# Kernel tuning notes

Measured on AMD Instinct MI355X. Metric: run time of the kernel, lower is better.

The kernel has to match this reference:

```python
import jax, jax.numpy as jnp
import numpy as np

N = 100000
IN_DIM = 256
HID = 128
E = 1600000


def _gcn_conv(x, W, b, src, dst, n_nodes):
    """PyG GCNConv: add self-loops, symmetric normalization, linear transform."""
    xw = x @ W  # [N, H]
    loop = jnp.arange(n_nodes, dtype=src.dtype)
    s = jnp.concatenate([src, loop])  # sources (j)
    d = jnp.concatenate([dst, loop])  # targets (i)
    ones = jnp.ones(s.shape[0], dtype=x.dtype)
    deg = jax.ops.segment_sum(ones, d, num_segments=n_nodes)  # in-degree incl. self-loop
    dinv = jnp.where(deg > 0, jax.lax.rsqrt(deg), 0.0)
    norm = dinv[s] * dinv[d]  # [E+N]
    msgs = xw[s] * norm[:, None]  # gather + scale
    out = jax.ops.segment_sum(msgs, d, num_segments=n_nodes)  # scatter-add at targets
    return out + b


def setup_inputs() -> dict:
    key = jax.random.key(0)
    ks = jax.random.split(key, 12)
    x = jax.random.normal(ks[0], (N, IN_DIM), dtype=jnp.float32)
    edge_index = jax.random.randint(ks[1], (2, E), 0, N, dtype=jnp.int64)
    h_node = jax.random.uniform(ks[2], (N,), dtype=jnp.float32)
    # learned params (glorot-ish scale)
    W1 = jax.random.normal(ks[3], (IN_DIM, HID), dtype=jnp.float32) / np.sqrt(IN_DIM)
    b1 = jnp.zeros((HID,), dtype=jnp.float32)
    W2 = jax.random.normal(ks[4], (HID, HID), dtype=jnp.float32) / np.sqrt(HID)
    b2 = jnp.zeros((HID,), dtype=jnp.float32)
    Wc = jax.random.normal(ks[5], (HID, 2), dtype=jnp.float32) / np.sqrt(HID)
    bc = jnp.zeros((2,), dtype=jnp.float32)
    Wf = jax.random.normal(ks[6], (HID, 2), dtype=jnp.float32) / np.sqrt(HID)
    bf = jnp.zeros((2,), dtype=jnp.float32)
    return {"x": x, "edge_index": edge_index, "h_node": h_node,
            "W1": W1, "b1": b1, "W2": W2, "b2": b2,
            "Wc": Wc, "bc": bc, "Wf": Wf, "bf": bf}


def reference(x, edge_index, h_node, W1, b1, W2, b2, Wc, bc, Wf, bf):
    src, dst = edge_index[0], edge_index[1]
    h1 = jax.nn.relu(_gcn_conv(x, W1, b1, src, dst, x.shape[0]))      # [N, HID]
    logits_coarse = h1 @ Wc + bc                                      # [N, 2]
    alpha = h_node[:, None]                                           # [N, 1]
    h2 = jax.nn.relu(_gcn_conv(h1, W2, b2, src, dst, x.shape[0]))     # [N, HID]
    h2_adaptive = alpha * h2 + (1.0 - alpha) * h1
    logits_fine = h2_adaptive @ Wf + bf                               # [N, 2]
    return 0.5 * logits_coarse + 0.5 * logits_fine
```

## Files before the change

kernel.cpp:

```cpp
#include <hip/hip_runtime.h>


#define HID 128
#define SHIFT 9
#define RANGE 512
#define MAXB 256
#define TILE 4096

typedef __bf16 bf16x8 __attribute__((ext_vector_type(8)));
typedef float  f32x4  __attribute__((ext_vector_type(4)));
typedef float  f32x2  __attribute__((ext_vector_type(2)));

__device__ __forceinline__ unsigned short f2bf(float x) {
    unsigned int b = __float_as_uint(x);
    b += 0x7fffu + ((b >> 16) & 1u);
    return (unsigned short)(b >> 16);
}
__device__ __forceinline__ float bflo(unsigned int u) { return __uint_as_float(u << 16); }
__device__ __forceinline__ float bfhi(unsigned int u) { return __uint_as_float(u & 0xffff0000u); }
__device__ __forceinline__ unsigned packbf(float a, float b) {
    return (unsigned)f2bf(a) | ((unsigned)f2bf(b) << 16);
}


__global__ __launch_bounds__(256)
void bincount_kernel(const int* __restrict__ dst, int* __restrict__ bin_counts,
                     int E, int NB) {
    __shared__ int h[MAXB];
    for (int i = threadIdx.x; i < NB; i += 256) h[i] = 0;
    __syncthreads();
    const int base = blockIdx.x * TILE;
#pragma unroll
    for (int j = 0; j < TILE; j += 256) {
        int e = base + j + threadIdx.x;
        if (e < E) atomicAdd(&h[((unsigned)dst[e]) >> SHIFT], 1);
    }
    __syncthreads();
    for (int i = threadIdx.x; i < NB; i += 256) {
        int v = h[i];
        if (v) atomicAdd(&bin_counts[i], v);
    }
}

__global__ void binscan_kernel(const int* __restrict__ bin_counts,
                               int* __restrict__ bin_off, int* __restrict__ bin_cur, int NB) {
    __shared__ int sh[MAXB];
    const int t = threadIdx.x;
    int v = (t < NB) ? bin_counts[t] : 0;
    sh[t] = v;
    __syncthreads();
    for (int s = 1; s < 256; s <<= 1) {
        int x = (t >= s) ? sh[t - s] : 0;
        __syncthreads();
        sh[t] += x;
        __syncthreads();
    }
    if (t < NB) {
        int ex = sh[t] - v;
        bin_off[t] = ex;
        bin_cur[t] = ex;
    }
}

__global__ __launch_bounds__(256)
void stage_kernel(const int* __restrict__ src, const int* __restrict__ dst,
                  int* __restrict__ bin_cur, unsigned* __restrict__ pairs, int E) {
    __shared__ int sh_hist[MAXB];
    __shared__ int sh_off[MAXB];
    __shared__ int sh_ex[MAXB];
    __shared__ int sh_gbase[MAXB];
    __shared__ uint2 stg[TILE];
    const int t = threadIdx.x;
    const int base = blockIdx.x * TILE;
    const int cnt = min(TILE, E - base);

    for (int i = t; i < MAXB; i += 256) sh_hist[i] = 0;
    __syncthreads();

    int s[16], d[16], r[16];
#pragma unroll
    for (int j = 0; j < 16; ++j) {
        const int k = j * 256 + t;
        if (k < cnt) {
            s[j] = src[base + k];
            d[j] = dst[base + k];
            r[j] = atomicAdd(&sh_hist[((unsigned)d[j]) >> SHIFT], 1);
        }
    }
    __syncthreads();

    const int hv = sh_hist[t];
    sh_off[t] = hv;
    __syncthreads();
    for (int st = 1; st < 256; st <<= 1) {
        int x = (t >= st) ? sh_off[t - st] : 0;
        __syncthreads();
        sh_off[t] += x;
        __syncthreads();
    }
    sh_ex[t] = sh_off[t] - hv;
    if (hv > 0) sh_gbase[t] = atomicAdd(&bin_cur[t], hv);
    __syncthreads();

#pragma unroll
    for (int j = 0; j < 16; ++j) {
        const int k = j * 256 + t;
        if (k < cnt) {
            int b = ((unsigned)d[j]) >> SHIFT;
            stg[sh_ex[b] + r[j]] = make_uint2((unsigned)s[j], (unsigned)d[j]);
        }
    }
    __syncthreads();

    for (int i = t; i < cnt; i += 256) {
        uint2 p = stg[i];
        int b = (int)(p.y >> SHIFT);
        unsigned w = ((p.y & (RANGE - 1)) << 23) | p.x;
        pairs[sh_gbase[b] + (i - sh_ex[b])] = w;
    }
}

__global__ __launch_bounds__(256)
void binrowp_kernel(const unsigned* __restrict__ pairs, const int* __restrict__ bin_off,
                    float* __restrict__ dinv, int* __restrict__ rowp,
                    int N, int NB, int E) {
    __shared__ int c[RANGE];
    __shared__ int sh[256];
    const int b = blockIdx.x;
    const int t = threadIdx.x;
    const int nb = b << SHIFT;
    const int nr = min(RANGE, N - nb);
    for (int i = t; i < RANGE; i += 256) c[i] = 0;
    __syncthreads();
    const int lo = bin_off[b];
    const int hi = (b + 1 < NB) ? bin_off[b + 1] : E;
    for (int i = lo + t; i < hi; i += 256)
        atomicAdd(&c[pairs[i] >> 23], 1);
    __syncthreads();
    const int v0 = c[2 * t], v1 = c[2 * t + 1];
    const int pr = v0 + v1;
    sh[t] = pr;
    __syncthreads();
    for (int s = 1; s < 256; s <<= 1) {
        int x = (t >= s) ? sh[t - s] : 0;
        __syncthreads();
        sh[t] += x;
        __syncthreads();
    }
    const int ex = sh[t] - pr + lo;
    if (2 * t < nr) {
        rowp[nb + 2 * t] = ex;
        dinv[nb + 2 * t] = rsqrtf((float)(v0 + 1));
    }
    if (2 * t + 1 < nr) {
        rowp[nb + 2 * t + 1] = ex + v0;
        dinv[nb + 2 * t + 1] = rsqrtf((float)(v1 + 1));
    }
    if (b == 0 && t == 0) rowp[N] = E;
}

__global__ __launch_bounds__(256)
void fine_kernel(const unsigned* __restrict__ pairs, const int* __restrict__ bin_off,
                 const int* __restrict__ rowp, const float* __restrict__ dinv,
                 unsigned* __restrict__ colv1, int N, int NB, int E) {
    __shared__ int cur[RANGE];
    const int b = blockIdx.x;
    const int nb = b << SHIFT;
    const int nr = min(RANGE, N - nb);
    for (int i = threadIdx.x; i < nr; i += 256) cur[i] = rowp[nb + i];
    __syncthreads();
    const int lo = bin_off[b];
    const int hi = (b + 1 < NB) ? bin_off[b + 1] : E;
    for (int i = lo + threadIdx.x; i < hi; i += 256) {
        unsigned w = pairs[i];
        unsigned s = w & 0x7fffffu;
        int pos = atomicAdd(&cur[w >> 23], 1);
        unsigned w15 = __float2uint_rn(dinv[s] * 32767.0f);
        colv1[pos] = (s << 15) | w15;
    }
}

__global__ void prep_kernel(const float* __restrict__ W1, const float* __restrict__ W2,
                            unsigned short* __restrict__ wt1, unsigned short* __restrict__ wt2,
                            int K1, int* __restrict__ bin_counts) {
    int idx = blockIdx.x * 256 + threadIdx.x;
    if (idx < MAXB) bin_counts[idx] = 0;
    if (idx < 128 * K1) {
        int nn = idx / K1, k = idx - nn * K1;
        wt1[(size_t)nn * K1 + k] = f2bf(W1[(size_t)k * 128 + nn]);
    }
    if (idx < 128 * 128) {
        int nn = idx >> 7, k = idx & 127;
        wt2[(size_t)nn * 128 + k] = f2bf(W2[(size_t)k * 128 + nn]);
    }
}

template <bool A_BF16, int K>
__global__ __launch_bounds__(256)
void gemm_kernel(const void* __restrict__ Aptr, const unsigned short* __restrict__ Wt,
                 unsigned short* __restrict__ Out, int nrows) {
    constexpr int NIT = K / 32;
    constexpr int DEPTH = (NIT < 4) ? NIT : 4;
    const int tid  = threadIdx.x;
    const int wave = tid >> 6;
    const int lane = tid & 63;
    const int q = lane >> 4;
    const int r = lane & 15;
    const int wrow = blockIdx.x * 128 + wave * 32;
    const size_t row0 = (size_t)min(wrow + r,      nrows - 1);
    const size_t row1 = (size_t)min(wrow + 16 + r, nrows - 1);

    const unsigned short* A16 = (const unsigned short*)Aptr;
    const float*          A32 = (const float*)Aptr;

    f32x4 acc[2][8];
#pragma unroll
    for (int s = 0; s < 2; ++s)
#pragma unroll
        for (int c = 0; c < 8; ++c) acc[s][c] = (f32x4){0.f, 0.f, 0.f, 0.f};

    bf16x8 preb[DEPTH][2];
    float4 pref[DEPTH][2][2];

#pragma unroll
    for (int i = 0; i < DEPTH; ++i) {
        const int kk = i * 32 + q * 8;
        if (A_BF16) {
            preb[i][0] = *reinterpret_cast<const bf16x8*>(A16 + row0 * K + kk);
            preb[i][1] = *reinterpret_cast<const bf16x8*>(A16 + row1 * K + kk);
        } else {
            pref[i][0][0] = *reinterpret_cast<const float4*>(A32 + row0 * K + kk);
            pref[i][0][1] = *reinterpret_cast<const float4*>(A32 + row0 * K + kk + 4);
            pref[i][1][0] = *reinterpret_cast<const float4*>(A32 + row1 * K + kk);
            pref[i][1][1] = *reinterpret_cast<const float4*>(A32 + row1 * K + kk + 4);
        }
    }

#pragma unroll
    for (int it = 0; it < NIT; ++it) {
        const int slot = it % DEPTH;
        const int kk = it * 32 + q * 8;

        bf16x8 bfr[8];
#pragma unroll
        for (int c = 0; c < 8; ++c)
            bfr[c] = *reinterpret_cast<const bf16x8*>(Wt + (size_t)(c * 16 + r) * K + kk);

        bf16x8 afrag[2];
#pragma unroll
        for (int s = 0; s < 2; ++s) {
            if (A_BF16) {
                afrag[s] = preb[slot][s];
            } else {
                const float4 x0 = pref[slot][s][0];
                const float4 x1 = pref[slot][s][1];
                bf16x8 a;
                a[0] = (__bf16)x0.x; a[1] = (__bf16)x0.y; a[2] = (__bf16)x0.z; a[3] = (__bf16)x0.w;
                a[4] = (__bf16)x1.x; a[5] = (__bf16)x1.y; a[6] = (__bf16)x1.z; a[7] = (__bf16)x1.w;
                afrag[s] = a;
            }
        }

        if (it + DEPTH < NIT) {
            const int kk2 = (it + DEPTH) * 32 + q * 8;
            if (A_BF16) {
                preb[slot][0] = *reinterpret_cast<const bf16x8*>(A16 + row0 * K + kk2);
                preb[slot][1] = *reinterpret_cast<const bf16x8*>(A16 + row1 * K + kk2);
            } else {
                pref[slot][0][0] = *reinterpret_cast<const float4*>(A32 + row0 * K + kk2);
                pref[slot][0][1] = *reinterpret_cast<const float4*>(A32 + row0 * K + kk2 + 4);
                pref[slot][1][0] = *reinterpret_cast<const float4*>(A32 + row1 * K + kk2);
                pref[slot][1][1] = *reinterpret_cast<const float4*>(A32 + row1 * K + kk2 + 4);
            }
        }

#pragma unroll
        for (int c = 0; c < 8; ++c) {
            acc[0][c] = __builtin_amdgcn_mfma_f32_16x16x32_bf16(afrag[0], bfr[c], acc[0][c], 0, 0, 0);
            acc[1][c] = __builtin_amdgcn_mfma_f32_16x16x32_bf16(afrag[1], bfr[c], acc[1][c], 0, 0, 0);
        }
    }

#pragma unroll
    for (int s = 0; s < 2; ++s)
#pragma unroll
        for (int v = 0; v < 4; ++v) {
            const int row = wrow + s * 16 + q * 4 + v;
            if (row < nrows) {
#pragma unroll
                for (int c = 0; c < 8; ++c)
                    Out[(size_t)row * 128 + c * 16 + r] = f2bf(acc[s][c][v]);
            }
        }
}


#define AGG_ISSUE(g, TBL)                                                     \
    if ((g) * 4 < cnt) {                                                      \
        _Pragma("unroll")                                                     \
        for (int j = 0; j < 4; ++j) {                                         \
            const int sl = (g) * 4 + j;                                       \
            const unsigned cg = (unsigned)__shfl((int)cw, qb + sl);           \
            wt[sl] = (float)(cg & 0x7fffu) * (1.0f / 32767.0f);               \
            pf[sl] = *reinterpret_cast<const uint4*>(                         \
                (const char*)(TBL) + (((cg >> 15) << 8) + coff));             \
        }                                                                     \
    }

#define AGG_CONS(g)                                                          \
    if ((g) * 4 < cnt) {                                                     \
        _Pragma("unroll")                                                    \
        for (int j = 0; j < 4; ++j) {                                        \
            const int sl = (g) * 4 + j;                                      \
            const float w = wt[sl];                                          \
            const uint4 uu = pf[sl];                                         \
            A0 += (f32x2){bflo(uu.x), bfhi(uu.x)} * w;                       \
            A1 += (f32x2){bflo(uu.y), bfhi(uu.y)} * w;                       \
            A2 += (f32x2){bflo(uu.z), bfhi(uu.z)} * w;                       \
            A3 += (f32x2){bflo(uu.w), bfhi(uu.w)} * w;                       \
        }                                                                    \
    }

#define AGG_EDGE_LOOP(TBL)                                                   \
    unsigned cw = (beg + c < end) ? colv1[beg + c] : 0u;                     \
    for (int base = beg; base < end; base += 16) {                           \
        const int cnt = end - base;                                          \
        AGG_ISSUE(0, TBL) AGG_ISSUE(1, TBL) AGG_ISSUE(2, TBL) AGG_ISSUE(3, TBL) \
        unsigned cw_next = 0u;                                               \
        if (base + 16 + c < end) cw_next = colv1[base + 16 + c];             \
        AGG_CONS(0) AGG_CONS(1) AGG_CONS(2) AGG_CONS(3)                      \
        cw = cw_next;                                                        \
    }

__global__ __launch_bounds__(256)
void agg1_kernel(const unsigned short* __restrict__ xw, const unsigned* __restrict__ colv1,
                 const int* __restrict__ rowp, const float* __restrict__ dinv,
                 const float* __restrict__ b1, const float* __restrict__ Wc,
                 const float* __restrict__ bc, uint4* __restrict__ h1,
                 float* __restrict__ outp, int n) {
    const int node = blockIdx.x * 16 + (threadIdx.x >> 4);
    if (node >= n) return;
    const int lane = threadIdx.x & 63;
    const int c    = lane & 15;
    const int qb   = lane & 48;
    const unsigned coff = (unsigned)c << 4;
    const float di = dinv[node];
    const int beg = rowp[node], end = rowp[node + 1];

    const uint4 su = *reinterpret_cast<const uint4*>(
        (const char*)xw + (((unsigned)node << 8) + coff));

    f32x2 A0 = {0.f,0.f}, A1 = {0.f,0.f}, A2 = {0.f,0.f}, A3 = {0.f,0.f};
    uint4 pf[16];
    float wt[16];

    AGG_EDGE_LOOP(xw)

    A0 += (f32x2){bflo(su.x), bfhi(su.x)} * di;
    A1 += (f32x2){bflo(su.y), bfhi(su.y)} * di;
    A2 += (f32x2){bflo(su.z), bfhi(su.z)} * di;
    A3 += (f32x2){bflo(su.w), bfhi(su.w)} * di;

    const float4 bb0 = reinterpret_cast<const float4*>(b1)[2*c];
    const float4 bb1 = reinterpret_cast<const float4*>(b1)[2*c + 1];
    float a0 = fmaxf(A0[0]*di + bb0.x, 0.f), a1 = fmaxf(A0[1]*di + bb0.y, 0.f);
    float a2 = fmaxf(A1[0]*di + bb0.z, 0.f), a3 = fmaxf(A1[1]*di + bb0.w, 0.f);
    float a4 = fmaxf(A2[0]*di + bb1.x, 0.f), a5 = fmaxf(A2[1]*di + bb1.y, 0.f);
    float a6 = fmaxf(A3[0]*di + bb1.z, 0.f), a7 = fmaxf(A3[1]*di + bb1.w, 0.f);

    h1[((unsigned)node << 4) + c] =
        make_uint4(packbf(a0,a1), packbf(a2,a3), packbf(a4,a5), packbf(a6,a7));

    const float4 w0 = reinterpret_cast<const float4*>(Wc)[4*c];
    const float4 w1 = reinterpret_cast<const float4*>(Wc)[4*c + 1];
    const float4 w2 = reinterpret_cast<const float4*>(Wc)[4*c + 2];
    const float4 w3 = reinterpret_cast<const float4*>(Wc)[4*c + 3];
    float c0 = a0*w0.x + a1*w0.z + a2*w1.x + a3*w1.z
             + a4*w2.x + a5*w2.z + a6*w3.x + a7*w3.z;
    float c1 = a0*w0.y + a1*w0.w + a2*w1.y + a3*w1.w
             + a4*w2.y + a5*w2.w + a6*w3.y + a7*w3.w;
#pragma unroll
    for (int off = 1; off < 16; off <<= 1) {
        c0 += __shfl_xor(c0, off);
        c1 += __shfl_xor(c1, off);
    }
    if (c == 0) {
        outp[2 * (size_t)node]     = 0.5f * (c0 + bc[0]);
        outp[2 * (size_t)node + 1] = 0.5f * (c1 + bc[1]);
    }
}

__global__ __launch_bounds__(256)
void agg2_kernel(const unsigned short* __restrict__ xw2, const uint4* __restrict__ h1,
                 const unsigned* __restrict__ colv1, const int* __restrict__ rowp,
                 const float* __restrict__ dinv, const float* __restrict__ b2,
                 const float* __restrict__ Wf, const float* __restrict__ bfv,
                 const float* __restrict__ hnode, float* __restrict__ outp, int n) {
    const int node = blockIdx.x * 16 + (threadIdx.x >> 4);
    if (node >= n) return;
    const int lane = threadIdx.x & 63;
    const int c    = lane & 15;
    const int qb   = lane & 48;
    const unsigned coff = (unsigned)c << 4;
    const float di = dinv[node];
    const int beg = rowp[node], end = rowp[node + 1];

    const uint4 su = *reinterpret_cast<const uint4*>(
        (const char*)xw2 + (((unsigned)node << 8) + coff));

    f32x2 A0 = {0.f,0.f}, A1 = {0.f,0.f}, A2 = {0.f,0.f}, A3 = {0.f,0.f};
    uint4 pf[16];
    float wt[16];

    AGG_EDGE_LOOP(xw2)

    A0 += (f32x2){bflo(su.x), bfhi(su.x)} * di;
    A1 += (f32x2){bflo(su.y), bfhi(su.y)} * di;
    A2 += (f32x2){bflo(su.z), bfhi(su.z)} * di;
    A3 += (f32x2){bflo(su.w), bfhi(su.w)} * di;

    const float4 bb0 = reinterpret_cast<const float4*>(b2)[2*c];
    const float4 bb1 = reinterpret_cast<const float4*>(b2)[2*c + 1];
    float h20 = fmaxf(A0[0]*di + bb0.x, 0.f), h21 = fmaxf(A0[1]*di + bb0.y, 0.f);
    float h22 = fmaxf(A1[0]*di + bb0.z, 0.f), h23 = fmaxf(A1[1]*di + bb0.w, 0.f);
    float h24 = fmaxf(A2[0]*di + bb1.x, 0.f), h25 = fmaxf(A2[1]*di + bb1.y, 0.f);
    float h26 = fmaxf(A3[0]*di + bb1.z, 0.f), h27 = fmaxf(A3[1]*di + bb1.w, 0.f);

    const float alpha = hnode[node];
    const float beta  = 1.f - alpha;
    const uint4 hh = h1[((unsigned)node << 4) + c];
    const float ha0 = alpha*h20 + beta*bflo(hh.x);
    const float ha1 = alpha*h21 + beta*bfhi(hh.x);
    const float ha2 = alpha*h22 + beta*bflo(hh.y);
    const float ha3 = alpha*h23 + beta*bfhi(hh.y);
    const float ha4 = alpha*h24 + beta*bflo(hh.z);
    const float ha5 = alpha*h25 + beta*bfhi(hh.z);
    const float ha6 = alpha*h26 + beta*bflo(hh.w);
    const float ha7 = alpha*h27 + beta*bfhi(hh.w);

    const float4 w0 = reinterpret_cast<const float4*>(Wf)[4*c];
    const float4 w1 = reinterpret_cast<const float4*>(Wf)[4*c + 1];
    const float4 w2 = reinterpret_cast<const float4*>(Wf)[4*c + 2];
    const float4 w3 = reinterpret_cast<const float4*>(Wf)[4*c + 3];
    float f0 = ha0*w0.x + ha1*w0.z + ha2*w1.x + ha3*w1.z
             + ha4*w2.x + ha5*w2.z + ha6*w3.x + ha7*w3.z;
    float f1 = ha0*w0.y + ha1*w0.w + ha2*w1.y + ha3*w1.w
             + ha4*w2.y + ha5*w2.w + ha6*w3.y + ha7*w3.w;
#pragma unroll
    for (int off = 1; off < 16; off <<= 1) {
        f0 += __shfl_xor(f0, off);
        f1 += __shfl_xor(f1, off);
    }
    if (c == 0) {
        outp[2 * (size_t)node]     += 0.5f * (f0 + bfv[0]);
        outp[2 * (size_t)node + 1] += 0.5f * (f1 + bfv[1]);
    }
}


extern "C" void kernel_launch(void* const* d_in, const int* in_sizes, int n_in,
                              void* d_out, int out_size, void* d_ws, size_t ws_size,
                              hipStream_t stream) {
    const float* x     = (const float*)d_in[0];
    const int*   ei    = (const int*)d_in[1];
    const float* hnode = (const float*)d_in[2];
    const float* W1    = (const float*)d_in[3];
    const float* b1    = (const float*)d_in[4];
    const float* W2    = (const float*)d_in[5];
    const float* b2    = (const float*)d_in[6];
    const float* Wc    = (const float*)d_in[7];
    const float* bc    = (const float*)d_in[8];
    const float* Wf    = (const float*)d_in[9];
    const float* bfv   = (const float*)d_in[10];

    const int N  = in_sizes[2];
    const int E  = in_sizes[1] / 2;
    const int K1 = in_sizes[3] / HID;
    const int NB = (N + RANGE - 1) >> SHIFT;
    const int* srcv = ei;
    const int* dstv = ei + E;
    float* outp = (float*)d_out;

    char* ws = (char*)d_ws;
    size_t off = 0;
    auto alloc = [&](size_t bytes) -> char* {
        char* p = ws + off;
        off += (bytes + 255) & ~(size_t)255;
        return p;
    };
    unsigned short* xw       = (unsigned short*)alloc((size_t)N * HID * 2);
    unsigned short* h1       = (unsigned short*)alloc((size_t)N * HID * 2);
    float*          dinv     = (float*)alloc((size_t)N * 4);
    int*            rowp     = (int*)alloc((size_t)(N + 1) * 4);
    unsigned*       colv1    = (unsigned*)alloc((size_t)E * 4);
    unsigned*       pairs    = (unsigned*)alloc((size_t)E * 4);
    int*            bin_counts = (int*)alloc(MAXB * 4);
    int*            bin_off    = (int*)alloc(MAXB * 4);
    int*            bin_cur    = (int*)alloc(MAXB * 4);
    unsigned short* wt1      = (unsigned short*)alloc((size_t)HID * K1 * 2);
    unsigned short* wt2      = (unsigned short*)alloc((size_t)HID * HID * 2);

    prep_kernel<<<(HID * K1 + 255) / 256, 256, 0, stream>>>(W1, W2, wt1, wt2, K1, bin_counts);

    const int ntiles = (E + TILE - 1) / TILE;
    bincount_kernel<<<ntiles, 256, 0, stream>>>(dstv, bin_counts, E, NB);
    binscan_kernel<<<1, 256, 0, stream>>>(bin_counts, bin_off, bin_cur, NB);
    stage_kernel<<<ntiles, 256, 0, stream>>>(srcv, dstv, bin_cur, pairs, E);
    binrowp_kernel<<<NB, 256, 0, stream>>>(pairs, bin_off, dinv, rowp, N, NB, E);
    fine_kernel<<<NB, 256, 0, stream>>>(pairs, bin_off, rowp, dinv, colv1, N, NB, E);

    gemm_kernel<false, 256><<<(N + 127) / 128, 256, 0, stream>>>((const void*)x, wt1, xw, N);
    agg1_kernel<<<(N + 15) / 16, 256, 0, stream>>>(xw, colv1, rowp, dinv,
                                                   b1, Wc, bc, (uint4*)h1, outp, N);
    gemm_kernel<true, 128><<<(N + 127) / 128, 256, 0, stream>>>((const void*)h1, wt2, xw, N);
    agg2_kernel<<<(N + 15) / 16, 256, 0, stream>>>(xw, (const uint4*)h1, colv1,
                                                   rowp, dinv, b2, Wf, bfv, hnode, outp, N);
}
```

Baseline: 402.6 us.

## Stage GEMM weights in swizzled LDS and halve rows per block

The dense GEMM kernel now loads the transposed bf16 weight matrix cooperatively into shared memory, XOR-swizzled to avoid bank conflicts, in K-halves for the 256-wide layer. Each wave reads B fragments from LDS instead of global memory. Each wave now handles 16 rows instead of 32, so blocks cover 64 rows and the grid doubles. This is meant to cut redundant global/L2 weight traffic and register pressure, at the cost of more blocks re-staging weights and added barriers. An unused f32x2 shfl_xor helper is also added.

After: 375.8 us. -6.7%, faster.

```diff
diff --git a/kernel.cpp b/kernel.cpp
--- a/kernel.cpp
+++ b/kernel.cpp
@@ -199,99 +199,106 @@
 __global__ __launch_bounds__(256)
 void gemm_kernel(const void* __restrict__ Aptr, const unsigned short* __restrict__ Wt,
                  unsigned short* __restrict__ Out, int nrows) {
-    constexpr int NIT = K / 32;
+    constexpr int NIT  = K / 32;
     constexpr int DEPTH = (NIT < 4) ? NIT : 4;
+    constexpr int HK   = (K > 128) ? (K / 2) : K;
+    constexpr int CHH  = HK / 8;
+    constexpr int PH   = K / HK;
+    constexpr int NITP = HK / 32;
+    __shared__ uint4 sB[128 * CHH];
+
     const int tid  = threadIdx.x;
     const int wave = tid >> 6;
     const int lane = tid & 63;
     const int q = lane >> 4;
     const int r = lane & 15;
-    const int wrow = blockIdx.x * 128 + wave * 32;
-    const size_t row0 = (size_t)min(wrow + r,      nrows - 1);
-    const size_t row1 = (size_t)min(wrow + 16 + r, nrows - 1);
+
+    const int wrow = blockIdx.x * 64 + wave * 16;
+    const size_t row0 = (size_t)min(wrow + r, nrows - 1);
 
     const unsigned short* A16 = (const unsigned short*)Aptr;
     const float*          A32 = (const float*)Aptr;
 
-    f32x4 acc[2][8];
-#pragma unroll
-    for (int s = 0; s < 2; ++s)
-#pragma unroll
-        for (int c = 0; c < 8; ++c) acc[s][c] = (f32x4){0.f, 0.f, 0.f, 0.f};
-
-    bf16x8 preb[DEPTH][2];
-    float4 pref[DEPTH][2][2];
+    f32x4 acc[8];
+#pragma unroll
+    for (int c = 0; c < 8; ++c) acc[c] = (f32x4){0.f, 0.f, 0.f, 0.f};
+
+    bf16x8 preb[DEPTH];
+    float4 pref[DEPTH][2];
 
 #pragma unroll
     for (int i = 0; i < DEPTH; ++i) {
         const int kk = i * 32 + q * 8;
         if (A_BF16) {
-            preb[i][0] = *reinterpret_cast<const bf16x8*>(A16 + row0 * K + kk);
-            preb[i][1] = *reinterpret_cast<const bf16x8*>(A16 + row1 * K + kk);
+            preb[i] = *reinterpret_cast<const bf16x8*>(A16 + row0 * K + kk);
         } else {
-            pref[i][0][0] = *reinterpret_cast<const float4*>(A32 + row0 * K + kk);
-            pref[i][0][1] = *reinterpret_cast<const float4*>(A32 + row0 * K + kk + 4);
-            pref[i][1][0] = *reinterpret_cast<const float4*>(A32 + row1 * K + kk);
-            pref[i][1][1] = *reinterpret_cast<const float4*>(A32 + row1 * K + kk + 4);
+            pref[i][0] = *reinterpret_cast<const float4*>(A32 + row0 * K + kk);
+            pref[i][1] = *reinterpret_cast<const float4*>(A32 + row0 * K + kk + 4);
         }
     }
 
 #pragma unroll
-    for (int it = 0; it < NIT; ++it) {
-        const int slot = it % DEPTH;
-        const int kk = it * 32 + q * 8;
-
-        bf16x8 bfr[8];
-#pragma unroll
-        for (int c = 0; c < 8; ++c)
-            bfr[c] = *reinterpret_cast<const bf16x8*>(Wt + (size_t)(c * 16 + r) * K + kk);
-
-        bf16x8 afrag[2];
-#pragma unroll
-        for (int s = 0; s < 2; ++s) {
+    for (int ph = 0; ph < PH; ++ph) {
+        if (ph) __syncthreads();
+        for (int idx = tid; idx < 128 * CHH; idx += 256) {
+            const int col = idx / CHH;
+            const int kc  = idx & (CHH - 1);
+            const uint4 v = *reinterpret_cast<const uint4*>(
+                Wt + (size_t)col * K + ph * HK + kc * 8);
+            sB[col * CHH + (kc ^ (col & (CHH - 1)))] = v;
+        }
+        __syncthreads();
+
+#pragma unroll
+        for (int itp = 0; itp < NITP; ++itp) {
+            const int git  = ph * NITP + itp;
+            const int slot = git % DEPTH;
+
+            bf16x8 bcur[8];
+#pragma unroll
+            for (int c = 0; c < 8; ++c) {
+                const int col = c * 16 + r;
+                const int chunk = (itp * 4 + q) ^ (col & (CHH - 1));
+                bcur[c] = *reinterpret_cast<const bf16x8*>(&sB[col * CHH + chunk]);
+            }
+
+            bf16x8 afrag;
             if (A_BF16) {
-                afrag[s] = preb[slot][s];
+                afrag = preb[slot];
             } else {
-                const float4 x0 = pref[slot][s][0];
-                const float4 x1 = pref[slot][s][1];
+                const float4 x0 = pref[slot][0];
+                const float4 x1 = pref[slot][1];
                 bf16x8 a;
                 a[0] = (__bf16)x0.x; a[1] = (__bf16)x0.y; a[2] = (__bf16)x0.z; a[3] = (__bf16)x0.w;
                 a[4] = (__bf16)x1.x; a[5] = (__bf16)x1.y; a[6] = (__bf16)x1.z; a[7] = (__bf16)x1.w;
-                afrag[s] = a;
+                afrag = a;
             }
+
+            if (git + DEPTH < NIT) {
+                const int kk2 = (git + DEPTH) * 32 + q * 8;
+                if (A_BF16) {
+                    preb[slot] = *reinterpret_cast<const bf16x8*>(A16 + row0 * K + kk2);
+                } else {
+                    pref[slot][0] = *reinterpret_cast<const float4*>(A32 + row0 * K + kk2);
+                    pref[slot][1] = *reinterpret_cast<const float4*>(A32 + row0 * K + kk2 + 4);
+                }
+            }
+
+#pragma unroll
+            for (int c = 0; c < 8; ++c)
+                acc[c] = __builtin_amdgcn_mfma_f32_16x16x32_bf16(afrag, bcur[c], acc[c], 0, 0, 0);
         }
-
-        if (it + DEPTH < NIT) {
-            const int kk2 = (it + DEPTH) * 32 + q * 8;
-            if (A_BF16) {
-                preb[slot][0] = *reinterpret_cast<const bf16x8*>(A16 + row0 * K + kk2);
-                preb[slot][1] = *reinterpret_cast<const bf16x8*>(A16 + row1 * K + kk2);
-            } else {
-                pref[slot][0][0] = *reinterpret_cast<const float4*>(A32 + row0 * K + kk2);
-                pref[slot][0][1] = *reinterpret_cast<const float4*>(A32 + row0 * K + kk2 + 4);
-                pref[slot][1][0] = *reinterpret_cast<const float4*>(A32 + row1 * K + kk2);
-                pref[slot][1][1] = *reinterpret_cast<const float4*>(A32 + row1 * K + kk2 + 4);
-            }
+    }
+
+#pragma unroll
+    for (int v = 0; v < 4; ++v) {
+        const int row = wrow + q * 4 + v;
+        if (row < nrows) {
+#pragma unroll
+            for (int c = 0; c < 8; ++c)
+                Out[(size_t)row * 128 + c * 16 + r] = f2bf(acc[c][v]);
         }
-
-#pragma unroll
-        for (int c = 0; c < 8; ++c) {
-            acc[0][c] = __builtin_amdgcn_mfma_f32_16x16x32_bf16(afrag[0], bfr[c], acc[0][c], 0, 0, 0);
-            acc[1][c] = __builtin_amdgcn_mfma_f32_16x16x32_bf16(afrag[1], bfr[c], acc[1][c], 0, 0, 0);
-        }
-    }
-
-#pragma unroll
-    for (int s = 0; s < 2; ++s)
-#pragma unroll
-        for (int v = 0; v < 4; ++v) {
-            const int row = wrow + s * 16 + q * 4 + v;
-            if (row < nrows) {
-#pragma unroll
-                for (int c = 0; c < 8; ++c)
-                    Out[(size_t)row * 128 + c * 16 + r] = f2bf(acc[s][c][v]);
-            }
-        }
+    }
 }
 
 
@@ -331,6 +338,10 @@
         AGG_CONS(0) AGG_CONS(1) AGG_CONS(2) AGG_CONS(3)                      \
         cw = cw_next;                                                        \
     }
+
+__device__ __forceinline__ f32x2 __shfl_xor(f32x2 v, int m) {
+    return (f32x2){__shfl_xor(v[0], m), __shfl_xor(v[1], m)};
+}
 
 __global__ __launch_bounds__(256)
 void agg1_kernel(const unsigned short* __restrict__ xw, const unsigned* __restrict__ colv1,
@@ -509,10 +520,10 @@
     binrowp_kernel<<<NB, 256, 0, stream>>>(pairs, bin_off, dinv, rowp, N, NB, E);
     fine_kernel<<<NB, 256, 0, stream>>>(pairs, bin_off, rowp, dinv, colv1, N, NB, E);
 
-    gemm_kernel<false, 256><<<(N + 127) / 128, 256, 0, stream>>>((const void*)x, wt1, xw, N);
+    gemm_kernel<false, 256><<<(N + 63) / 64, 256, 0, stream>>>((const void*)x, wt1, xw, N);
     agg1_kernel<<<(N + 15) / 16, 256, 0, stream>>>(xw, colv1, rowp, dinv,
                                                    b1, Wc, bc, (uint4*)h1, outp, N);
-    gemm_kernel<true, 128><<<(N + 127) / 128, 256, 0, stream>>>((const void*)h1, wt2, xw, N);
+    gemm_kernel<true, 128><<<(N + 63) / 64, 256, 0, stream>>>((const void*)h1, wt2, xw, N);
     agg2_kernel<<<(N + 15) / 16, 256, 0, stream>>>(xw, (const uint4*)h1, colv1,
                                                    rowp, dinv, b2, Wf, bfv, hnode, outp, N);
 }
```
